# Optimization experiments

Measured on AMD Instinct MI355X. Metric: run time of the kernel, lower is better.

Reference implementation:

```python
import jax, jax.numpy as jnp
import numpy as np

N = 500_000   # total nodes
D = 256       # in_dim
G = 1024      # num graphs (segments)
H = max(32, D // 2)  # gate hidden = 128
L = D // 2    # local pool dim = 128


def setup_inputs() -> dict:
    key = jax.random.key(0)
    ks = jax.random.split(key, 8)
    x = jax.random.normal(ks[0], (N, D), dtype=jnp.float32)
    batch = jnp.sort(jax.random.randint(ks[1], (N,), 0, G, dtype=jnp.int32))
    s = 0.02
    w1 = jax.random.normal(ks[2], (D, H), dtype=jnp.float32) * s
    b1 = jnp.zeros((H,), dtype=jnp.float32)
    w2 = jax.random.normal(ks[3], (H, 1), dtype=jnp.float32) * s
    b2 = jnp.zeros((1,), dtype=jnp.float32)
    lp_w = jax.random.normal(ks[4], (D, L), dtype=jnp.float32) * s
    lp_b = jnp.zeros((L,), dtype=jnp.float32)
    return {"x": x, "batch": batch, "w1": w1, "b1": b1, "w2": w2,
            "b2": b2, "lp_w": lp_w, "lp_b": lp_b}


def reference(x, batch, w1, b1, w2, b2, lp_w, lp_b):
    # segment counts (guard empty segments)
    ones = jnp.ones((x.shape[0],), dtype=x.dtype)
    cnt = jax.ops.segment_sum(ones, batch, num_segments=G)
    cnt = jnp.maximum(cnt, 1.0)[:, None]                      # [G,1]

    # mean pool
    mean_p = jax.ops.segment_sum(x, batch, num_segments=G) / cnt

    # max pool
    max_p = jax.ops.segment_max(x, batch, num_segments=G)

    # global attention pool: gate MLP -> per-segment softmax -> weighted sum
    # (Dropout is identity at inference.)
    h = jax.nn.gelu(x @ w1 + b1, approximate=False)           # [N,H]
    gate = (h @ w2 + b2)[:, 0]                                # [N]
    gmax = jax.ops.segment_max(gate, batch, num_segments=G)   # [G]
    e = jnp.exp(gate - gmax[batch])                           # [N]
    denom = jax.ops.segment_sum(e, batch, num_segments=G)     # [G]
    a = e / denom[batch]                                      # [N] softmax per graph
    att_p = jax.ops.segment_sum(a[:, None] * x, batch, num_segments=G)

    # local MLP pool then mean
    local = jax.nn.gelu(x @ lp_w + lp_b, approximate=False)   # [N,L]
    local_mean = jax.ops.segment_sum(local, batch, num_segments=G) / cnt

    return jnp.concatenate([mean_p, max_p, att_p, local_mean], axis=-1)  # [G, 3D + D//2]
```

## Files before the change

kernel.cpp:

```cpp
#include <hip/hip_runtime.h>
#include <hip/hip_bf16.h>
#include <float.h>
#include <math.h>


typedef __bf16 bf16;
typedef __bf16 bf16x4 __attribute__((ext_vector_type(4)));
typedef __bf16 bf16x8 __attribute__((ext_vector_type(8)));
typedef float f32x4 __attribute__((ext_vector_type(4)));

#define D 256
#define HDIM 128
#define LDIM 128

__device__ __forceinline__ float gelu_f(float v) {
    return 0.5f * v * (1.0f + erff(v * 0.70710678118654752f));
}

__global__ __launch_bounds__(256) void k_prep(const float* __restrict__ w1,
                                              const float* __restrict__ lpw,
                                              bf16* __restrict__ w1T,
                                              bf16* __restrict__ lpT,
                                              float* __restrict__ local_sum,
                                              int* __restrict__ segstart,
                                              int G, int N) {
    int t = blockIdx.x * 256 + threadIdx.x;
    if (t == 0) segstart[G] = N;
    if (t < G * LDIM) local_sum[t] = 0.0f;
    if (t < HDIM * D) {
        int n = t >> 8;
        int k = t & 255;
        w1T[t] = (bf16)w1[k * HDIM + n];
        lpT[t] = (bf16)lpw[k * LDIM + n];
    }
}

__global__ __launch_bounds__(256, 3) void k_gate_local(
    const float* __restrict__ x, const int* __restrict__ batch,
    const bf16* __restrict__ w1T, const float* __restrict__ b1,
    const float* __restrict__ w2, const float* __restrict__ b2,
    const bf16* __restrict__ lpT, const float* __restrict__ lpb,
    float* __restrict__ gate, float* __restrict__ local_sum, int N)
{
    __shared__ bf16 xs[64][264];
    __shared__ int bs[64];
    __shared__ float gpart[4][64];

    const int tid  = threadIdx.x;
    const int wave = tid >> 6;
    const int lane = tid & 63;
    const int quad = lane >> 4;
    const int l16  = lane & 15;
    const long base = (long)blockIdx.x * 64;

    #pragma unroll
    for (int it = 0; it < 16; ++it) {
        int idx = it * 256 + tid;
        int row = idx >> 6;
        int c4  = idx & 63;
        long node = base + row;
        float4 v;
        if (node < N) v = *(const float4*)(x + node * D + c4 * 4);
        else          v = make_float4(0.f, 0.f, 0.f, 0.f);
        bf16x4 pk;
        pk[0] = (bf16)v.x; pk[1] = (bf16)v.y; pk[2] = (bf16)v.z; pk[3] = (bf16)v.w;
        *(bf16x4*)(&xs[row][c4 * 4]) = pk;
    }
    if (tid < 64) bs[tid] = (base + tid < N) ? batch[base + tid] : 0x7fffffff;
    __syncthreads();

    const int c0 = wave * 32 + l16;
    const int c1 = c0 + 16;

    f32x4 zero = {0.f, 0.f, 0.f, 0.f};
    f32x4 h0[4], h1[4], l0[4], l1[4];
    #pragma unroll
    for (int mt = 0; mt < 4; ++mt) { h0[mt] = zero; h1[mt] = zero; l0[mt] = zero; l1[mt] = zero; }

    #pragma unroll
    for (int kt = 0; kt < 8; ++kt) {
        int k0 = kt * 32 + quad * 8;
        bf16x8 bw0 = *(const bf16x8*)(w1T + c0 * D + k0);
        bf16x8 bw1 = *(const bf16x8*)(w1T + c1 * D + k0);
        bf16x8 bp0 = *(const bf16x8*)(lpT + c0 * D + k0);
        bf16x8 bp1 = *(const bf16x8*)(lpT + c1 * D + k0);
        #pragma unroll
        for (int mt = 0; mt < 4; ++mt) {
            bf16x8 a = *(const bf16x8*)(&xs[mt * 16 + l16][k0]);
            h0[mt] = __builtin_amdgcn_mfma_f32_16x16x32_bf16(a, bw0, h0[mt], 0, 0, 0);
            h1[mt] = __builtin_amdgcn_mfma_f32_16x16x32_bf16(a, bw1, h1[mt], 0, 0, 0);
            l0[mt] = __builtin_amdgcn_mfma_f32_16x16x32_bf16(a, bp0, l0[mt], 0, 0, 0);
            l1[mt] = __builtin_amdgcn_mfma_f32_16x16x32_bf16(a, bp1, l1[mt], 0, 0, 0);
        }
    }

    {
        const float b1c0 = b1[c0], b1c1 = b1[c1];
        const float w2c0 = w2[c0], w2c1 = w2[c1];
        #pragma unroll
        for (int mt = 0; mt < 4; ++mt) {
            #pragma unroll
            for (int r = 0; r < 4; ++r) {
                float v = gelu_f(h0[mt][r] + b1c0) * w2c0
                        + gelu_f(h1[mt][r] + b1c1) * w2c1;
                v += __shfl_down(v, 8, 16);
                v += __shfl_down(v, 4, 16);
                v += __shfl_down(v, 2, 16);
                v += __shfl_down(v, 1, 16);
                if (l16 == 0) gpart[wave][mt * 16 + quad * 4 + r] = v;
            }
        }
    }
    __syncthreads();
    if (tid < 64) {
        long node = base + tid;
        if (node < N)
            gate[node] = gpart[0][tid] + gpart[1][tid] + gpart[2][tid] + gpart[3][tid] + b2[0];
    }

    const float lb0 = lpb[c0], lb1 = lpb[c1];
    const bool fast = (base + 63 < N) && (bs[0] == bs[63]);
    if (fast) {
        float s0 = 0.f, s1 = 0.f;
        #pragma unroll
        for (int mt = 0; mt < 4; ++mt) {
            #pragma unroll
            for (int r = 0; r < 4; ++r) {
                s0 += gelu_f(l0[mt][r] + lb0);
                s1 += gelu_f(l1[mt][r] + lb1);
            }
        }
        s0 += __shfl_xor(s0, 16); s0 += __shfl_xor(s0, 32);
        s1 += __shfl_xor(s1, 16); s1 += __shfl_xor(s1, 32);
        if (quad == 0) {
            int g = bs[0];
            atomicAdd(&local_sum[g * LDIM + c0], s0);
            atomicAdd(&local_sum[g * LDIM + c1], s1);
        }
    } else {
        int cur = -1;
        float s0 = 0.f, s1 = 0.f;
        #pragma unroll
        for (int mt = 0; mt < 4; ++mt) {
            #pragma unroll
            for (int r = 0; r < 4; ++r) {
                int lrow = mt * 16 + quad * 4 + r;
                if (base + lrow < N) {
                    int g = bs[lrow];
                    if (g != cur) {
                        if (cur >= 0) {
                            atomicAdd(&local_sum[cur * LDIM + c0], s0);
                            atomicAdd(&local_sum[cur * LDIM + c1], s1);
                        }
                        cur = g; s0 = 0.f; s1 = 0.f;
                    }
                    s0 += gelu_f(l0[mt][r] + lb0);
                    s1 += gelu_f(l1[mt][r] + lb1);
                }
            }
        }
        if (cur >= 0) {
            atomicAdd(&local_sum[cur * LDIM + c0], s0);
            atomicAdd(&local_sum[cur * LDIM + c1], s1);
        }
    }
}

__device__ __forceinline__ int lower_bound_i(const int* a, int n, int v) {
    int lo = 0, hi = n;
    while (lo < hi) { int mid = (lo + hi) >> 1; if (a[mid] < v) lo = mid + 1; else hi = mid; }
    return lo;
}

__global__ __launch_bounds__(256) void k_stats(
    const int* __restrict__ batch, const float* __restrict__ gate,
    float* __restrict__ aw, float* __restrict__ segdenom,
    int* __restrict__ segstart, int N)
{
    const int g   = blockIdx.x;
    const int tid = threadIdx.x;
    const int wave = tid >> 6;
    const int lane = tid & 63;

    __shared__ int sse[2];
    __shared__ float wred[4];

    if (tid == 0) sse[0] = lower_bound_i(batch, N, g);
    if (tid == 1) sse[1] = lower_bound_i(batch, N, g + 1);
    __syncthreads();
    const int start = sse[0], end = sse[1];
    if (tid == 0) segstart[g] = start;

    float m = -FLT_MAX;
    for (int i = start + tid; i < end; i += 256) m = fmaxf(m, gate[i]);
    #pragma unroll
    for (int off = 32; off > 0; off >>= 1) m = fmaxf(m, __shfl_xor(m, off));
    if (lane == 0) wred[wave] = m;
    __syncthreads();
    m = fmaxf(fmaxf(wred[0], wred[1]), fmaxf(wred[2], wred[3]));
    __syncthreads();

    float s = 0.f;
    for (int i = start + tid; i < end; i += 256) {
        float e = expf(gate[i] - m);
        aw[i] = e;
        s += e;
    }
    #pragma unroll
    for (int off = 32; off > 0; off >>= 1) s += __shfl_xor(s, off);
    if (lane == 0) wred[wave] = s;
    __syncthreads();
    if (tid == 0) segdenom[g] = wred[0] + wred[1] + wred[2] + wred[3];
}

__global__ __launch_bounds__(256) void k_pool(
    const float* __restrict__ x,
    const float* __restrict__ aw, const float* __restrict__ segdenom,
    const int* __restrict__ segstart, const float* __restrict__ local_sum,
    float* __restrict__ out)
{
    const int g    = blockIdx.x >> 1;
    const int half = blockIdx.x & 1;
    const int tid  = threadIdx.x;
    const int rg   = tid >> 5;
    const int c4   = tid & 31;

    __shared__ float psum[8][128];
    __shared__ float pmax[8][128];
    __shared__ float patt[8][128];

    const int start = segstart[g];
    const int end   = segstart[g + 1];
    const int cnt   = end - start;

    const float* xb = x + half * 128 + c4 * 4;

    float sx = 0, sy = 0, sz = 0, sw = 0;
    float ax = 0, ay = 0, az = 0, aw4 = 0;
    float mx = -FLT_MAX, my = -FLT_MAX, mz = -FLT_MAX, mw = -FLT_MAX;

    int i = start + rg;
    #define POOL_BODY(ri)                                                    \
        {                                                                    \
            float e = aw[ri];                                                \
            float4 v = *(const float4*)(xb + (long)(ri) * D);                \
            sx += v.x; sy += v.y; sz += v.z; sw += v.w;                      \
            ax += e * v.x; ay += e * v.y; az += e * v.z; aw4 += e * v.w;     \
            mx = fmaxf(mx, v.x); my = fmaxf(my, v.y);                        \
            mz = fmaxf(mz, v.z); mw = fmaxf(mw, v.w);                        \
        }
    for (; i + 8 < end; i += 16) { POOL_BODY(i); POOL_BODY(i + 8); }
    if (i < end) POOL_BODY(i);
    #undef POOL_BODY

    const int cb = c4 * 4;
    psum[rg][cb] = sx; psum[rg][cb+1] = sy; psum[rg][cb+2] = sz; psum[rg][cb+3] = sw;
    patt[rg][cb] = ax; patt[rg][cb+1] = ay; patt[rg][cb+2] = az; patt[rg][cb+3] = aw4;
    pmax[rg][cb] = mx; pmax[rg][cb+1] = my; pmax[rg][cb+2] = mz; pmax[rg][cb+3] = mw;
    __syncthreads();

    const float inv  = 1.0f / fmaxf((float)cnt, 1.0f);
    const float dn   = segdenom[g];
    const float invd = (dn > 0.f) ? 1.0f / dn : 0.f;
    const long  o    = (long)g * 896;

    if (tid < 128) {
        int c = tid;
        float s = 0.f, a = 0.f, mm = -FLT_MAX;
        #pragma unroll
        for (int r = 0; r < 8; ++r) {
            s += psum[r][c];
            a += patt[r][c];
            mm = fmaxf(mm, pmax[r][c]);
        }
        if (cnt == 0) mm = -INFINITY;
        out[o + half * 128 + c]       = s * inv;
        out[o + 256 + half * 128 + c] = mm;
        out[o + 512 + half * 128 + c] = a * invd;
        if (half == 1) out[o + 768 + c] = local_sum[g * LDIM + c] * inv;
    }
}

extern "C" void kernel_launch(void* const* d_in, const int* in_sizes, int n_in,
                              void* d_out, int out_size, void* d_ws, size_t ws_size,
                              hipStream_t stream) {
    const float* x   = (const float*)d_in[0];
    const int* batch = (const int*)d_in[1];
    const float* w1  = (const float*)d_in[2];
    const float* b1  = (const float*)d_in[3];
    const float* w2  = (const float*)d_in[4];
    const float* b2  = (const float*)d_in[5];
    const float* lpw = (const float*)d_in[6];
    const float* lpb = (const float*)d_in[7];
    float* out = (float*)d_out;

    const int N = in_sizes[0] / D;
    const int G = out_size / 896;

    char* ws = (char*)d_ws;
    size_t off = 0;
    float* gate      = (float*)(ws + off); off += (((size_t)N * 4) + 255) & ~(size_t)255;
    float* aw        = (float*)(ws + off); off += (((size_t)N * 4) + 255) & ~(size_t)255;
    bf16*  w1T       = (bf16*)(ws + off);  off += (size_t)HDIM * D * 2;
    bf16*  lpT       = (bf16*)(ws + off);  off += (size_t)LDIM * D * 2;
    float* local_sum = (float*)(ws + off); off += (size_t)G * LDIM * 4;
    float* segdenom  = (float*)(ws + off); off += (size_t)G * 4;
    int*   segstart  = (int*)(ws + off);   off += (size_t)(G + 1) * 4;

    const int prep_threads = G * LDIM;
    k_prep<<<(prep_threads + 255) / 256, 256, 0, stream>>>(w1, lpw, w1T, lpT, local_sum,
                                                           segstart, G, N);
    k_gate_local<<<(int)((N + 63) / 64), 256, 0, stream>>>(x, batch, w1T, b1, w2, b2,
                                                           lpT, lpb, gate, local_sum, N);
    k_stats<<<G, 256, 0, stream>>>(batch, gate, aw, segdenom, segstart, N);
    k_pool<<<2 * G, 256, 0, stream>>>(x, aw, segdenom, segstart, local_sum, out);
}
```

Measured before the change: 884.3 us.

## Fuse gate MLP, online softmax and all pooling into one per-segment kernel

Replaces the three-kernel pipeline (gate/local matmul with atomics, per-segment softmax stats, pooling) with a single kernel that assigns one block per graph. Each block streams its segment in 48-row chunks, keeping the chunk in fp32 shared memory. Mean, max, attention-weighted and local-MLP sums are all accumulated from that one pass, using an online softmax with a running max and rescaled denominator. This removes the second full read of x, the gate and weight buffers in global memory, and the atomics, at the cost of only G blocks with a serial chunk loop and larger fp32 shared memory, which limits occupancy and load/compute overlap.

```diff
diff --git a/kernel.cpp b/kernel.cpp
--- a/kernel.cpp
+++ b/kernel.cpp
@@ -5,13 +5,15 @@
 
 
 typedef __bf16 bf16;
-typedef __bf16 bf16x4 __attribute__((ext_vector_type(4)));
 typedef __bf16 bf16x8 __attribute__((ext_vector_type(8)));
 typedef float f32x4 __attribute__((ext_vector_type(4)));
 
 #define D 256
 #define HDIM 128
 #define LDIM 128
+#define ROWS 48
+#define XPAD 260
+#define NMT 3
 
 __device__ __forceinline__ float gelu_f(float v) {
     return 0.5f * v * (1.0f + erff(v * 0.70710678118654752f));
@@ -20,13 +22,8 @@
 __global__ __launch_bounds__(256) void k_prep(const float* __restrict__ w1,
                                               const float* __restrict__ lpw,
                                               bf16* __restrict__ w1T,
-                                              bf16* __restrict__ lpT,
-                                              float* __restrict__ local_sum,
-                                              int* __restrict__ segstart,
-                                              int G, int N) {
+                                              bf16* __restrict__ lpT) {
     int t = blockIdx.x * 256 + threadIdx.x;
-    if (t == 0) segstart[G] = N;
-    if (t < G * LDIM) local_sum[t] = 0.0f;
     if (t < HDIM * D) {
         int n = t >> 8;
         int k = t & 255;
@@ -35,70 +32,111 @@
     }
 }
 
-__global__ __launch_bounds__(256, 3) void k_gate_local(
+__device__ __forceinline__ int lower_bound_i(const int* a, int n, int v) {
+    int lo = 0, hi = n;
+    while (lo < hi) { int mid = (lo + hi) >> 1; if (a[mid] < v) lo = mid + 1; else hi = mid; }
+    return lo;
+}
+
+__global__ __launch_bounds__(256, 3) void k_fused(
     const float* __restrict__ x, const int* __restrict__ batch,
     const bf16* __restrict__ w1T, const float* __restrict__ b1,
     const float* __restrict__ w2, const float* __restrict__ b2,
     const bf16* __restrict__ lpT, const float* __restrict__ lpb,
-    float* __restrict__ gate, float* __restrict__ local_sum, int N)
+    float* __restrict__ out, int N)
 {
-    __shared__ bf16 xs[64][264];
-    __shared__ int bs[64];
+    __shared__ float xs[ROWS][XPAD];
     __shared__ float gpart[4][64];
-
+    __shared__ int sse[2];
+
+    const int g    = blockIdx.x;
     const int tid  = threadIdx.x;
     const int wave = tid >> 6;
     const int lane = tid & 63;
     const int quad = lane >> 4;
     const int l16  = lane & 15;
-    const long base = (long)blockIdx.x * 64;
-
-    #pragma unroll
-    for (int it = 0; it < 16; ++it) {
-        int idx = it * 256 + tid;
-        int row = idx >> 6;
-        int c4  = idx & 63;
-        long node = base + row;
-        float4 v;
-        if (node < N) v = *(const float4*)(x + node * D + c4 * 4);
-        else          v = make_float4(0.f, 0.f, 0.f, 0.f);
-        bf16x4 pk;
-        pk[0] = (bf16)v.x; pk[1] = (bf16)v.y; pk[2] = (bf16)v.z; pk[3] = (bf16)v.w;
-        *(bf16x4*)(&xs[row][c4 * 4]) = pk;
-    }
-    if (tid < 64) bs[tid] = (base + tid < N) ? batch[base + tid] : 0x7fffffff;
+
+    if (tid == 0) sse[0] = lower_bound_i(batch, N, g);
+    if (tid == 1) sse[1] = lower_bound_i(batch, N, g + 1);
     __syncthreads();
+    const int start = sse[0], end = sse[1];
+    const int cnt = end - start;
 
     const int c0 = wave * 32 + l16;
     const int c1 = c0 + 16;
-
-    f32x4 zero = {0.f, 0.f, 0.f, 0.f};
-    f32x4 h0[4], h1[4], l0[4], l1[4];
-    #pragma unroll
-    for (int mt = 0; mt < 4; ++mt) { h0[mt] = zero; h1[mt] = zero; l0[mt] = zero; l1[mt] = zero; }
-
-    #pragma unroll
-    for (int kt = 0; kt < 8; ++kt) {
-        int k0 = kt * 32 + quad * 8;
-        bf16x8 bw0 = *(const bf16x8*)(w1T + c0 * D + k0);
-        bf16x8 bw1 = *(const bf16x8*)(w1T + c1 * D + k0);
-        bf16x8 bp0 = *(const bf16x8*)(lpT + c0 * D + k0);
-        bf16x8 bp1 = *(const bf16x8*)(lpT + c1 * D + k0);
-        #pragma unroll
-        for (int mt = 0; mt < 4; ++mt) {
-            bf16x8 a = *(const bf16x8*)(&xs[mt * 16 + l16][k0]);
-            h0[mt] = __builtin_amdgcn_mfma_f32_16x16x32_bf16(a, bw0, h0[mt], 0, 0, 0);
-            h1[mt] = __builtin_amdgcn_mfma_f32_16x16x32_bf16(a, bw1, h1[mt], 0, 0, 0);
-            l0[mt] = __builtin_amdgcn_mfma_f32_16x16x32_bf16(a, bp0, l0[mt], 0, 0, 0);
-            l1[mt] = __builtin_amdgcn_mfma_f32_16x16x32_bf16(a, bp1, l1[mt], 0, 0, 0);
-        }
-    }
-
-    {
-        const float b1c0 = b1[c0], b1c1 = b1[c1];
-        const float w2c0 = w2[c0], w2c1 = w2[c1];
-        #pragma unroll
-        for (int mt = 0; mt < 4; ++mt) {
+    const float b1c0 = b1[c0], b1c1 = b1[c1];
+    const float w2c0 = w2[c0], w2c1 = w2[c1];
+    const float lb0  = lpb[c0], lb1 = lpb[c1];
+    const float b2c  = b2[0];
+
+    float msum0=0.f, msum1=0.f, msum2=0.f, msum3=0.f;
+    float mmax0=-FLT_MAX, mmax1=-FLT_MAX, mmax2=-FLT_MAX, mmax3=-FLT_MAX;
+    float asum0=0.f, asum1=0.f, asum2=0.f, asum3=0.f;
+    float ls0=0.f, ls1=0.f;
+    float m_run = -FLT_MAX, denom = 0.f;
+
+    const f32x4 zf = {0.f, 0.f, 0.f, 0.f};
+
+    for (int base = start; base < end; base += ROWS) {
+        const int vr = min(ROWS, end - base);
+        const float* xb = x + (long)base * D + (lane << 2);
+
+        if (vr == ROWS) {
+            #pragma unroll
+            for (int it = 0; it < 12; ++it) {
+                const int row = it * 4 + wave;
+                const float4 t4 = *(const float4*)(xb + row * D);
+                msum0 += t4.x; msum1 += t4.y; msum2 += t4.z; msum3 += t4.w;
+                mmax0 = fmaxf(mmax0, t4.x); mmax1 = fmaxf(mmax1, t4.y);
+                mmax2 = fmaxf(mmax2, t4.z); mmax3 = fmaxf(mmax3, t4.w);
+                f32x4 v; v[0]=t4.x; v[1]=t4.y; v[2]=t4.z; v[3]=t4.w;
+                *(f32x4*)(&xs[row][lane << 2]) = v;
+            }
+        } else {
+            #pragma unroll
+            for (int it = 0; it < 12; ++it) {
+                const int row = it * 4 + wave;
+                f32x4 v = zf;
+                if (row < vr) {
+                    const float4 t4 = *(const float4*)(xb + row * D);
+                    msum0 += t4.x; msum1 += t4.y; msum2 += t4.z; msum3 += t4.w;
+                    mmax0 = fmaxf(mmax0, t4.x); mmax1 = fmaxf(mmax1, t4.y);
+                    mmax2 = fmaxf(mmax2, t4.z); mmax3 = fmaxf(mmax3, t4.w);
+                    v[0]=t4.x; v[1]=t4.y; v[2]=t4.z; v[3]=t4.w;
+                }
+                *(f32x4*)(&xs[row][lane << 2]) = v;
+            }
+        }
+        __syncthreads();
+
+        f32x4 h0[NMT], h1[NMT], l0[NMT], l1[NMT];
+        #pragma unroll
+        for (int mt = 0; mt < NMT; ++mt) { h0[mt]=zf; h1[mt]=zf; l0[mt]=zf; l1[mt]=zf; }
+
+        #pragma unroll
+        for (int kt = 0; kt < 8; ++kt) {
+            const int k0 = kt * 32 + quad * 8;
+            const bf16x8 bw0 = *(const bf16x8*)(w1T + c0 * D + k0);
+            const bf16x8 bw1 = *(const bf16x8*)(w1T + c1 * D + k0);
+            const bf16x8 bp0 = *(const bf16x8*)(lpT + c0 * D + k0);
+            const bf16x8 bp1 = *(const bf16x8*)(lpT + c1 * D + k0);
+            #pragma unroll
+            for (int mt = 0; mt < NMT; ++mt) {
+                const float* xp = &xs[mt * 16 + l16][k0];
+                const f32x4 fa = *(const f32x4*)(xp);
+                const f32x4 fb = *(const f32x4*)(xp + 4);
+                bf16x8 a;
+                a[0]=(bf16)fa[0]; a[1]=(bf16)fa[1]; a[2]=(bf16)fa[2]; a[3]=(bf16)fa[3];
+                a[4]=(bf16)fb[0]; a[5]=(bf16)fb[1]; a[6]=(bf16)fb[2]; a[7]=(bf16)fb[3];
+                h0[mt] = __builtin_amdgcn_mfma_f32_16x16x32_bf16(a, bw0, h0[mt], 0, 0, 0);
+                h1[mt] = __builtin_amdgcn_mfma_f32_16x16x32_bf16(a, bw1, h1[mt], 0, 0, 0);
+                l0[mt] = __builtin_amdgcn_mfma_f32_16x16x32_bf16(a, bp0, l0[mt], 0, 0, 0);
+                l1[mt] = __builtin_amdgcn_mfma_f32_16x16x32_bf16(a, bp1, l1[mt], 0, 0, 0);
+            }
+        }
+
+        #pragma unroll
+        for (int mt = 0; mt < NMT; ++mt) {
             #pragma unroll
             for (int r = 0; r < 4; ++r) {
                 float v = gelu_f(h0[mt][r] + b1c0) * w2c0
@@ -110,174 +148,82 @@
                 if (l16 == 0) gpart[wave][mt * 16 + quad * 4 + r] = v;
             }
         }
+        __syncthreads();
+
+        float gv = -FLT_MAX;
+        if (lane < vr)
+            gv = gpart[0][lane] + gpart[1][lane] + gpart[2][lane] + gpart[3][lane] + b2c;
+        float cm = gv;
+        #pragma unroll
+        for (int off = 32; off > 0; off >>= 1) cm = fmaxf(cm, __shfl_xor(cm, off));
+        const float m_new = fmaxf(m_run, cm);
+        const float fr = expf(m_run - m_new);
+        const float ew = (lane < vr) ? expf(gv - m_new) : 0.f;
+        float se = ew;
+        #pragma unroll
+        for (int off = 32; off > 0; off >>= 1) se += __shfl_xor(se, off);
+        denom = denom * fr + se;
+        m_run = m_new;
+
+        if (vr == ROWS) {
+            #pragma unroll
+            for (int mt = 0; mt < NMT; ++mt)
+                #pragma unroll
+                for (int r = 0; r < 4; ++r) {
+                    ls0 += gelu_f(l0[mt][r] + lb0);
+                    ls1 += gelu_f(l1[mt][r] + lb1);
+                }
+        } else {
+            #pragma unroll
+            for (int mt = 0; mt < NMT; ++mt)
+                #pragma unroll
+                for (int r = 0; r < 4; ++r) {
+                    if (mt * 16 + quad * 4 + r < vr) {
+                        ls0 += gelu_f(l0[mt][r] + lb0);
+                        ls1 += gelu_f(l1[mt][r] + lb1);
+                    }
+                }
+        }
+
+        asum0 *= fr; asum1 *= fr; asum2 *= fr; asum3 *= fr;
+        #pragma unroll
+        for (int it = 0; it < 12; ++it) {
+            const int row = it * 4 + wave;
+            const float e = __shfl(ew, row);
+            const f32x4 v = *(const f32x4*)(&xs[row][lane << 2]);
+            asum0 += e * v[0]; asum1 += e * v[1];
+            asum2 += e * v[2]; asum3 += e * v[3];
+        }
+        __syncthreads();
+    }
+
+    ls0 += __shfl_xor(ls0, 16); ls0 += __shfl_xor(ls0, 32);
+    ls1 += __shfl_xor(ls1, 16); ls1 += __shfl_xor(ls1, 32);
+
+    const float inv  = 1.0f / fmaxf((float)cnt, 1.0f);
+    const float invd = (denom > 0.f) ? 1.0f / denom : 0.f;
+    const long  o    = (long)g * 896;
+
+    float* red = &xs[0][0];
+    const int cb = (wave << 8) + (lane << 2);
+    red[cb]        = msum0; red[cb+1]        = msum1; red[cb+2]        = msum2; red[cb+3]        = msum3;
+    red[1024 + cb] = asum0; red[1024 + cb+1] = asum1; red[1024 + cb+2] = asum2; red[1024 + cb+3] = asum3;
+    red[2048 + cb] = mmax0; red[2048 + cb+1] = mmax1; red[2048 + cb+2] = mmax2; red[2048 + cb+3] = mmax3;
+    if (quad == 0) {
+        out[o + 768 + c0] = ls0 * inv;
+        out[o + 768 + c1] = ls1 * inv;
     }
     __syncthreads();
-    if (tid < 64) {
-        long node = base + tid;
-        if (node < N)
-            gate[node] = gpart[0][tid] + gpart[1][tid] + gpart[2][tid] + gpart[3][tid] + b2[0];
-    }
-
-    const float lb0 = lpb[c0], lb1 = lpb[c1];
-    const bool fast = (base + 63 < N) && (bs[0] == bs[63]);
-    if (fast) {
-        float s0 = 0.f, s1 = 0.f;
-        #pragma unroll
-        for (int mt = 0; mt < 4; ++mt) {
-            #pragma unroll
-            for (int r = 0; r < 4; ++r) {
-                s0 += gelu_f(l0[mt][r] + lb0);
-                s1 += gelu_f(l1[mt][r] + lb1);
-            }
-        }
-        s0 += __shfl_xor(s0, 16); s0 += __shfl_xor(s0, 32);
-        s1 += __shfl_xor(s1, 16); s1 += __shfl_xor(s1, 32);
-        if (quad == 0) {
-            int g = bs[0];
-            atomicAdd(&local_sum[g * LDIM + c0], s0);
-            atomicAdd(&local_sum[g * LDIM + c1], s1);
-        }
-    } else {
-        int cur = -1;
-        float s0 = 0.f, s1 = 0.f;
-        #pragma unroll
-        for (int mt = 0; mt < 4; ++mt) {
-            #pragma unroll
-            for (int r = 0; r < 4; ++r) {
-                int lrow = mt * 16 + quad * 4 + r;
-                if (base + lrow < N) {
-                    int g = bs[lrow];
-                    if (g != cur) {
-                        if (cur >= 0) {
-                            atomicAdd(&local_sum[cur * LDIM + c0], s0);
-                            atomicAdd(&local_sum[cur * LDIM + c1], s1);
-                        }
-                        cur = g; s0 = 0.f; s1 = 0.f;
-                    }
-                    s0 += gelu_f(l0[mt][r] + lb0);
-                    s1 += gelu_f(l1[mt][r] + lb1);
-                }
-            }
-        }
-        if (cur >= 0) {
-            atomicAdd(&local_sum[cur * LDIM + c0], s0);
-            atomicAdd(&local_sum[cur * LDIM + c1], s1);
-        }
-    }
-}
-
-__device__ __forceinline__ int lower_bound_i(const int* a, int n, int v) {
-    int lo = 0, hi = n;
-    while (lo < hi) { int mid = (lo + hi) >> 1; if (a[mid] < v) lo = mid + 1; else hi = mid; }
-    return lo;
-}
-
-__global__ __launch_bounds__(256) void k_stats(
-    const int* __restrict__ batch, const float* __restrict__ gate,
-    float* __restrict__ aw, float* __restrict__ segdenom,
-    int* __restrict__ segstart, int N)
-{
-    const int g   = blockIdx.x;
-    const int tid = threadIdx.x;
-    const int wave = tid >> 6;
-    const int lane = tid & 63;
-
-    __shared__ int sse[2];
-    __shared__ float wred[4];
-
-    if (tid == 0) sse[0] = lower_bound_i(batch, N, g);
-    if (tid == 1) sse[1] = lower_bound_i(batch, N, g + 1);
-    __syncthreads();
-    const int start = sse[0], end = sse[1];
-    if (tid == 0) segstart[g] = start;
-
-    float m = -FLT_MAX;
-    for (int i = start + tid; i < end; i += 256) m = fmaxf(m, gate[i]);
-    #pragma unroll
-    for (int off = 32; off > 0; off >>= 1) m = fmaxf(m, __shfl_xor(m, off));
-    if (lane == 0) wred[wave] = m;
-    __syncthreads();
-    m = fmaxf(fmaxf(wred[0], wred[1]), fmaxf(wred[2], wred[3]));
-    __syncthreads();
-
-    float s = 0.f;
-    for (int i = start + tid; i < end; i += 256) {
-        float e = expf(gate[i] - m);
-        aw[i] = e;
-        s += e;
-    }
-    #pragma unroll
-    for (int off = 32; off > 0; off >>= 1) s += __shfl_xor(s, off);
-    if (lane == 0) wred[wave] = s;
-    __syncthreads();
-    if (tid == 0) segdenom[g] = wred[0] + wred[1] + wred[2] + wred[3];
-}
-
-__global__ __launch_bounds__(256) void k_pool(
-    const float* __restrict__ x,
-    const float* __restrict__ aw, const float* __restrict__ segdenom,
-    const int* __restrict__ segstart, const float* __restrict__ local_sum,
-    float* __restrict__ out)
-{
-    const int g    = blockIdx.x >> 1;
-    const int half = blockIdx.x & 1;
-    const int tid  = threadIdx.x;
-    const int rg   = tid >> 5;
-    const int c4   = tid & 31;
-
-    __shared__ float psum[8][128];
-    __shared__ float pmax[8][128];
-    __shared__ float patt[8][128];
-
-    const int start = segstart[g];
-    const int end   = segstart[g + 1];
-    const int cnt   = end - start;
-
-    const float* xb = x + half * 128 + c4 * 4;
-
-    float sx = 0, sy = 0, sz = 0, sw = 0;
-    float ax = 0, ay = 0, az = 0, aw4 = 0;
-    float mx = -FLT_MAX, my = -FLT_MAX, mz = -FLT_MAX, mw = -FLT_MAX;
-
-    int i = start + rg;
-    #define POOL_BODY(ri)                                                    \
-        {                                                                    \
-            float e = aw[ri];                                                \
-            float4 v = *(const float4*)(xb + (long)(ri) * D);                \
-            sx += v.x; sy += v.y; sz += v.z; sw += v.w;                      \
-            ax += e * v.x; ay += e * v.y; az += e * v.z; aw4 += e * v.w;     \
-            mx = fmaxf(mx, v.x); my = fmaxf(my, v.y);                        \
-            mz = fmaxf(mz, v.z); mw = fmaxf(mw, v.w);                        \
-        }
-    for (; i + 8 < end; i += 16) { POOL_BODY(i); POOL_BODY(i + 8); }
-    if (i < end) POOL_BODY(i);
-    #undef POOL_BODY
-
-    const int cb = c4 * 4;
-    psum[rg][cb] = sx; psum[rg][cb+1] = sy; psum[rg][cb+2] = sz; psum[rg][cb+3] = sw;
-    patt[rg][cb] = ax; patt[rg][cb+1] = ay; patt[rg][cb+2] = az; patt[rg][cb+3] = aw4;
-    pmax[rg][cb] = mx; pmax[rg][cb+1] = my; pmax[rg][cb+2] = mz; pmax[rg][cb+3] = mw;
-    __syncthreads();
-
-    const float inv  = 1.0f / fmaxf((float)cnt, 1.0f);
-    const float dn   = segdenom[g];
-    const float invd = (dn > 0.f) ? 1.0f / dn : 0.f;
-    const long  o    = (long)g * 896;
-
-    if (tid < 128) {
-        int c = tid;
-        float s = 0.f, a = 0.f, mm = -FLT_MAX;
-        #pragma unroll
-        for (int r = 0; r < 8; ++r) {
-            s += psum[r][c];
-            a += patt[r][c];
-            mm = fmaxf(mm, pmax[r][c]);
-        }
+    {
+        const int col = tid;
+        const float s = red[col]        + red[256 + col]  + red[512 + col]  + red[768 + col];
+        const float a = red[1024 + col] + red[1280 + col] + red[1536 + col] + red[1792 + col];
+        float mm = fmaxf(fmaxf(red[2048 + col], red[2304 + col]),
+                         fmaxf(red[2560 + col], red[2816 + col]));
         if (cnt == 0) mm = -INFINITY;
-        out[o + half * 128 + c]       = s * inv;
-        out[o + 256 + half * 128 + c] = mm;
-        out[o + 512 + half * 128 + c] = a * invd;
-        if (half == 1) out[o + 768 + c] = local_sum[g * LDIM + c] * inv;
+        out[o + col]       = s * inv;
+        out[o + 256 + col] = mm;
+        out[o + 512 + col] = a * invd;
     }
 }
 
@@ -298,20 +244,9 @@
     const int G = out_size / 896;
 
     char* ws = (char*)d_ws;
-    size_t off = 0;
-    float* gate      = (float*)(ws + off); off += (((size_t)N * 4) + 255) & ~(size_t)255;
-    float* aw        = (float*)(ws + off); off += (((size_t)N * 4) + 255) & ~(size_t)255;
-    bf16*  w1T       = (bf16*)(ws + off);  off += (size_t)HDIM * D * 2;
-    bf16*  lpT       = (bf16*)(ws + off);  off += (size_t)LDIM * D * 2;
-    float* local_sum = (float*)(ws + off); off += (size_t)G * LDIM * 4;
-    float* segdenom  = (float*)(ws + off); off += (size_t)G * 4;
-    int*   segstart  = (int*)(ws + off);   off += (size_t)(G + 1) * 4;
-
-    const int prep_threads = G * LDIM;
-    k_prep<<<(prep_threads + 255) / 256, 256, 0, stream>>>(w1, lpw, w1T, lpT, local_sum,
-                                                           segstart, G, N);
-    k_gate_local<<<(int)((N + 63) / 64), 256, 0, stream>>>(x, batch, w1T, b1, w2, b2,
-                                                           lpT, lpb, gate, local_sum, N);
-    k_stats<<<G, 256, 0, stream>>>(batch, gate, aw, segdenom, segstart, N);
-    k_pool<<<2 * G, 256, 0, stream>>>(x, aw, segdenom, segstart, local_sum, out);
-}
+    bf16* w1T = (bf16*)ws;
+    bf16* lpT = (bf16*)(ws + (size_t)HDIM * D * sizeof(bf16));
+
+    k_prep<<<(HDIM * D + 255) / 256, 256, 0, stream>>>(w1, lpw, w1T, lpT);
+    k_fused<<<G, 256, 0, stream>>>(x, batch, w1T, b1, w2, b2, lpT, lpb, out, N);
+}
```

Result: slower. 1.036 ms (+17.1%).
